# Kernel tuning notes

Measured on AMD Instinct MI355X. Metric: run time of the kernel, lower is better.

Reference implementation:

```python
import jax, jax.numpy as jnp
import numpy as np

EPS = 1e-6

def _layernorm(x, g, b):
    mu = jnp.mean(x, axis=-1, keepdims=True)
    var = jnp.mean(jnp.square(x - mu), axis=-1, keepdims=True)
    return (x - mu) * jax.lax.rsqrt(var + EPS) * g + b

def _mhsa(xq, xk, xv, mask, Wq, bq, Wk, bk, Wv, bv, Wo, bo, num_heads):
    B, Nq, D = xq.shape
    Nk = xk.shape[1]
    dh = D // num_heads
    # project then split heads: [B, N, D] -> [B, H, N, dh]
    def split(x, W, b, N):
        return (x @ W + b).reshape(B, N, num_heads, dh).transpose(0, 2, 1, 3)
    q = split(xq, Wq, bq, Nq)
    k = split(xk, Wk, bk, Nk)
    v = split(xv, Wv, bv, Nk)
    scores = jnp.einsum('bhnd,bhmd->bhnm', q, k) / jnp.sqrt(jnp.float32(dh))
    if mask is not None:
        scores = scores + mask * (-1e9)
    w = jax.nn.softmax(scores, axis=-1)
    out = jnp.einsum('bhnm,bhmd->bhnd', w, v)          # [B,H,Nq,dh]
    out = out.transpose(0, 2, 1, 3).reshape(B, Nq, D)  # concat heads
    return out @ Wo + bo

def setup_inputs() -> dict:
    B, N, D, FF = 2, 2048, 512, 2048
    key = jax.random.key(0)
    ks = jax.random.split(key, 32)
    std = 0.02
    p = {}
    p['inputs'] = jax.random.normal(ks[0], (B, N, D), jnp.float32)
    p['enc_output'] = jax.random.normal(ks[1], (B, N, D), jnp.float32)
    # causal look-ahead mask: 1 where masked (future positions)
    p['look_ahead_mask'] = jnp.triu(jnp.ones((N, N), jnp.float32), k=1)[None, None]
    p['padding_mask'] = jnp.zeros((B, 1, 1, N), jnp.float32)
    i = 2
    for pre in ('q1', 'k1', 'v1', 'o1', 'q2', 'k2', 'v2', 'o2'):
        p[pre + '_w'] = jax.random.normal(ks[i], (D, D), jnp.float32) * std; i += 1
        p[pre + '_b'] = jnp.zeros((D,), jnp.float32)
    p['f1_w'] = jax.random.normal(ks[i], (D, FF), jnp.float32) * std; i += 1
    p['f1_b'] = jnp.zeros((FF,), jnp.float32)
    p['f2_w'] = jax.random.normal(ks[i], (FF, D), jnp.float32) * std; i += 1
    p['f2_b'] = jnp.zeros((D,), jnp.float32)
    for ln in ('ln1', 'ln2', 'ln3'):
        p[ln + '_g'] = jnp.ones((D,), jnp.float32)
        p[ln + '_b'] = jnp.zeros((D,), jnp.float32)
    p['training'] = 0
    return p

def reference(inputs, enc_output, look_ahead_mask, padding_mask,
              q1_w, q1_b, k1_w, k1_b, v1_w, v1_b, o1_w, o1_b,
              q2_w, q2_b, k2_w, k2_b, v2_w, v2_b, o2_w, o2_b,
              f1_w, f1_b, f2_w, f2_b,
              ln1_g, ln1_b, ln2_g, ln2_b, ln3_g, ln3_b,
              training):
    H = 8
    # self-attention (q=k=v=inputs), causal mask; dropout inactive (eval)
    attn1 = _mhsa(inputs, inputs, inputs, look_ahead_mask,
                  q1_w, q1_b, k1_w, k1_b, v1_w, v1_b, o1_w, o1_b, H)
    out1 = _layernorm(inputs + attn1, ln1_g, ln1_b)
    # cross attention: NOTE original arg order -> q=enc, k=enc, v=out1
    attn2 = _mhsa(enc_output, enc_output, out1, padding_mask,
                  q2_w, q2_b, k2_w, k2_b, v2_w, v2_b, o2_w, o2_b, H)
    out2 = _layernorm(out1 + attn2, ln2_g, ln2_b)
    ffn = jax.nn.relu(out2 @ f1_w + f1_b) @ f2_w + f2_b
    return _layernorm(out2 + ffn, ln3_g, ln3_b)
```

## Files before the change

### kernel.cpp

```cpp
#include <hip/hip_runtime.h>

typedef __attribute__((ext_vector_type(8))) _Float16 half8;
typedef __attribute__((ext_vector_type(4))) _Float16 half4;
typedef __attribute__((ext_vector_type(2))) _Float16 half2_t;
typedef __attribute__((ext_vector_type(2))) __fp16 fp16x2;
typedef __attribute__((ext_vector_type(4))) float f32x4;

#define AS1 __attribute__((address_space(1)))
#define AS3 __attribute__((address_space(3)))

constexpr int SEQ = 2048, DM = 512, FFD = 2048, NH = 8, DH = 64;
constexpr int M = 2 * SEQ;
constexpr float QSCALE = 0.125f * 1.4426950408889634f;

__global__ __launch_bounds__(256)
void preproc(const float* __restrict__ q1_w, const float* __restrict__ k1_w,
             const float* __restrict__ v1_w, const float* __restrict__ o1_w,
             const float* __restrict__ q2_w, const float* __restrict__ k2_w,
             const float* __restrict__ v2_w, const float* __restrict__ o2_w,
             const float* __restrict__ f1_w, const float* __restrict__ f2_w,
             _Float16* __restrict__ qk1t, _Float16* __restrict__ v1t,
             _Float16* __restrict__ o1t, _Float16* __restrict__ qk2t,
             _Float16* __restrict__ v2t, _Float16* __restrict__ o2t,
             _Float16* __restrict__ f1t, _Float16* __restrict__ f2t,
             const float* __restrict__ q1_b, const float* __restrict__ k1_b,
             const float* __restrict__ q2_b, const float* __restrict__ k2_b,
             float* __restrict__ qk1b, float* __restrict__ qk2b,
             const float* __restrict__ inp, const float* __restrict__ enc,
             _Float16* __restrict__ xh, _Float16* __restrict__ eh) {
    __shared__ _Float16 tile[64 * 65];
    const int j = blockIdx.x, tid = threadIdx.x;
    if (j < 1024) {
        const float* src; _Float16* dst; int K, N, n0, k0;
        if (j < 512) {
            int w8 = j >> 6, t = j & 63;
            K = 512; N = 512; n0 = (t & 7) * 64; k0 = (t >> 3) * 64;
            switch (w8) {
                case 0: src = q1_w; dst = qk1t; break;
                case 1: src = k1_w; dst = qk1t + 512 * 512; break;
                case 2: src = v1_w; dst = v1t; break;
                case 3: src = o1_w; dst = o1t; break;
                case 4: src = q2_w; dst = qk2t; break;
                case 5: src = k2_w; dst = qk2t + 512 * 512; break;
                case 6: src = v2_w; dst = v2t; break;
                default: src = o2_w; dst = o2t; break;
            }
        } else if (j < 768) {
            int t = j - 512; K = 512; N = 2048;
            n0 = (t % 32) * 64; k0 = (t / 32) * 64; src = f1_w; dst = f1t;
        } else {
            int t = j - 768; K = 2048; N = 512;
            n0 = (t % 8) * 64; k0 = (t / 8) * 64; src = f2_w; dst = f2t;
        }
        int c = tid & 63, r4 = tid >> 6;
        for (int i = 0; i < 16; i++) {
            int r = r4 * 16 + i;
            tile[r * 65 + c] = (_Float16)src[(size_t)(k0 + r) * N + n0 + c];
        }
        __syncthreads();
        for (int i = 0; i < 16; i++) {
            int r = r4 * 16 + i;
            dst[(size_t)(n0 + r) * K + k0 + c] = tile[c * 65 + r];
        }
    } else if (j == 1024) {
        for (int i = tid; i < 512; i += 256) { qk1b[i] = q1_b[i]; qk1b[512 + i] = k1_b[i]; }
    } else if (j == 1025) {
        for (int i = tid; i < 512; i += 256) { qk2b[i] = q2_b[i]; qk2b[512 + i] = k2_b[i]; }
    } else {
        int k = j - 1026;
        const float* s = (k < 1024) ? inp : enc;
        _Float16* d = (k < 1024) ? xh : eh;
        size_t base = (size_t)(k & 1023) * 2048 + tid * 8;
        f32x4 a = *(const f32x4*)(s + base);
        f32x4 b2 = *(const f32x4*)(s + base + 4);
        half8 h;
        h[0] = (_Float16)a[0]; h[1] = (_Float16)a[1];
        h[2] = (_Float16)a[2]; h[3] = (_Float16)a[3];
        h[4] = (_Float16)b2[0]; h[5] = (_Float16)b2[1];
        h[6] = (_Float16)b2[2]; h[7] = (_Float16)b2[3];
        *(half8*)(d + base) = h;
    }
}

template<int BM, int BN, int WM, int WN, bool RELU, int EPI, int SPLIT>
__global__ __launch_bounds__(256)
void gemm_tn(const _Float16* __restrict__ A, const _Float16* __restrict__ Bt,
             const float* __restrict__ bias,
             float* __restrict__ outF, _Float16* __restrict__ outH,
             _Float16* __restrict__ Qh, _Float16* __restrict__ Kh,
             const _Float16* __restrict__ A2, const _Float16* __restrict__ Bt2,
             const float* __restrict__ bias2,
             _Float16* __restrict__ Qh2, _Float16* __restrict__ Kh2,
             int Mtot, int N, int K) {
    constexpr int ROWS = BM + BN;
    __shared__ _Float16 smem[ROWS * 64];
    constexpr int AF = WM / 16, BF = WN / 16;
    constexpr int WROW = BM / WM;
    const int tid = threadIdx.x;
    const int wid = tid >> 6, lid = tid & 63;
    const int wr = (wid % WROW) * WM;
    const int wc = (wid / WROW) * WN;
    const int mi = lid & 15, qd = lid >> 4;
    const int gx = gridDim.x, gy = gridDim.y;
    const int L = blockIdx.y * gx + blockIdx.x;
    const int by = L % gy, bx = L / gy;
    const int m0 = by * BM, n0 = bx * BN;
    const int Kc = K / SPLIT;
    const int kbase = (SPLIT > 1) ? blockIdx.z * Kc : 0;
    const int job = (EPI == 4) ? blockIdx.z : 0;
    const _Float16* Ap = ((EPI == 4 && job) ? A2 : A) + (size_t)m0 * K + kbase;
    const _Float16* Bp = ((EPI == 4 && job) ? Bt2 : Bt) + (size_t)n0 * K + kbase;
    const float* bsel = (EPI == 4 && job) ? bias2 : bias;
    const int lrow = lid >> 3;
    const int gblk = (lid & 7) ^ ((lid >> 3) & 7);
    auto stage = [&](int kt) {
        #pragma unroll
        for (int l = 0; l < BM / 32; l++) {
            int c = l * 4 + wid;
            int row = c * 8 + lrow;
            __builtin_amdgcn_global_load_lds(
                (const AS1 unsigned int*)(Ap + (size_t)row * K + kt * 64 + gblk * 8),
                (AS3 unsigned int*)&smem[c * 512], 16, 0, 0);
        }
        #pragma unroll
        for (int l = 0; l < BN / 32; l++) {
            int c = l * 4 + wid;
            int row = c * 8 + lrow;
            __builtin_amdgcn_global_load_lds(
                (const AS1 unsigned int*)(Bp + (size_t)row * K + kt * 64 + gblk * 8),
                (AS3 unsigned int*)&smem[BM * 64 + c * 512], 16, 0, 0);
        }
    };
    f32x4 acc[AF][BF] = {};
    const int NIT = Kc / 64;
    stage(0);
    __builtin_amdgcn_s_waitcnt(0x0F70);
    __syncthreads();
    for (int t = 0; t < NIT; t++) {
        #pragma unroll
        for (int h = 0; h < 2; h++) {
            const int sA = ((4 * h + qd) ^ (mi & 7)) * 8;
            half8 af[AF], bfr[BF];
            #pragma unroll
            for (int i = 0; i < AF; i++)
                af[i] = *(const half8*)&smem[(wr + i * 16 + mi) * 64 + sA];
            #pragma unroll
            for (int j = 0; j < BF; j++)
                bfr[j] = *(const half8*)&smem[(BM + wc + j * 16 + mi) * 64 + sA];
            #pragma unroll
            for (int i = 0; i < AF; i++)
                #pragma unroll
                for (int j = 0; j < BF; j++)
                    acc[i][j] = __builtin_amdgcn_mfma_f32_16x16x32_f16(af[i], bfr[j], acc[i][j], 0, 0, 0);
        }
        if (t + 1 < NIT) {
            __syncthreads();
            stage(t + 1);
            __builtin_amdgcn_s_waitcnt(0x0F70);
            __syncthreads();
        }
    }
    float* oF = outF;
    if (SPLIT > 1 && outF) oF = outF + (size_t)blockIdx.z * Mtot * N;
    _Float16* oH = outH;
    if (EPI == 5) oH = outH + (size_t)blockIdx.z * Mtot * N;
    const bool doBias = bsel && (SPLIT == 1 || blockIdx.z == 0);
    #pragma unroll
    for (int i = 0; i < AF; i++) {
        #pragma unroll
        for (int j = 0; j < BF; j++) {
            #pragma unroll
            for (int r = 0; r < 4; r++) {
                int row = m0 + wr + i * 16 + qd * 4 + r;
                int col = n0 + wc + j * 16 + mi;
                float v = acc[i][j][r];
                if (EPI == 3) {
                    v += bsel[row];
                    outH[(size_t)row * N + col] = (_Float16)v;
                } else if (EPI == 4) {
                    if (doBias) v += bsel[col];
                    int hh = (col >> 6) & 7, d = col & 63;
                    int bb = row >> 11, n = row & 2047;
                    size_t idx = (((size_t)bb * 8 + hh) * SEQ + n) * 64 + d;
                    if (col < 512) (job ? Qh2 : Qh)[idx] = (_Float16)(v * QSCALE);
                    else           (job ? Kh2 : Kh)[idx] = (_Float16)v;
                } else if (EPI == 5) {
                    if (doBias) v += bsel[col];
                    oH[(size_t)row * N + col] = (_Float16)v;
                } else {
                    if (doBias) v += bsel[col];
                    if (RELU) v = fmaxf(v, 0.f);
                    size_t off = (size_t)row * N + col;
                    if (oF) oF[off] = v;
                    if (outH) outH[off] = (_Float16)v;
                }
            }
        }
    }
}

template<bool CAUSAL>
__global__ __launch_bounds__(256)
void attn_chunk(const _Float16* __restrict__ Qh, const _Float16* __restrict__ Kh,
                const _Float16* __restrict__ VT, int ldv,
                _Float16* __restrict__ Opart, float* __restrict__ Lpart) {
    const int qt = blockIdx.x, bh = blockIdx.y, c = blockIdx.z;
    int t0, stp, n;
    if (CAUSAL) {
        if (c > qt) return;
        t0 = c; stp = 4; n = (qt - c) / 4 + 1;
    } else {
        t0 = c * 8; stp = 1; n = 8;
    }
    __shared__ _Float16 QPs[64 * 64];
    __shared__ _Float16 Ks[2][64 * 64];
    __shared__ _Float16 Vs[2][64 * 64];
    const int tid = threadIdx.x, w = tid >> 6, lane = tid & 63;
    const int mi = lane & 15, qd = lane >> 4;
    const int qbase = qt * 64;
    const int b = bh >> 3, h = bh & 7;
    const _Float16* Qp = Qh + ((size_t)bh * SEQ + qbase) * 64;
    const _Float16* Kp = Kh + (size_t)bh * SEQ * 64;
    const _Float16* Vp = VT + (size_t)(h * 64) * ldv + (size_t)b * SEQ;
    const int r0 = tid >> 3, blk = tid & 7;
    const int sw = (blk ^ (r0 & 7)) * 8;
    const int lrow = lane >> 3;
    const int gblk = (lane & 7) ^ ((lane >> 3) & 7);
    const int f0 = (qd ^ (mi & 7)) * 8;
    const int f1 = ((qd + 4) ^ (mi & 7)) * 8;

    {
        half8 q0 = *(const half8*)(Qp + r0 * 64 + blk * 8);
        half8 q1 = *(const half8*)(Qp + (r0 + 32) * 64 + blk * 8);
        *(half8*)&QPs[r0 * 64 + sw] = q0;
        *(half8*)&QPs[(r0 + 32) * 64 + sw] = q1;
    }
    auto stageKV = [&](int t, int buf) {
        #pragma unroll
        for (int l = 0; l < 2; l++) {
            int cc = l * 4 + w;
            int row = cc * 8 + lrow;
            __builtin_amdgcn_global_load_lds(
                (const AS1 unsigned int*)(Kp + ((size_t)(t * 64 + row)) * 64 + gblk * 8),
                (AS3 unsigned int*)&Ks[buf][cc * 512], 16, 0, 0);
            __builtin_amdgcn_global_load_lds(
                (const AS1 unsigned int*)(Vp + (size_t)row * ldv + t * 64 + gblk * 8),
                (AS3 unsigned int*)&Vs[buf][cc * 512], 16, 0, 0);
        }
    };
    stageKV(t0, 0);
    __builtin_amdgcn_s_waitcnt(0x0F70);
    __syncthreads();
    half8 qb0 = *(half8*)&QPs[(w * 16 + mi) * 64 + f0];
    half8 qb1 = *(half8*)&QPs[(w * 16 + mi) * 64 + f1];
    f32x4 oacc[4] = {};
    float lacc = 0.f;
    for (int i = 0; i < n; i++) {
        const int t = t0 + i * stp;
        if (i + 1 < n) stageKV(t0 + (i + 1) * stp, (i + 1) & 1);
        const _Float16* ksb = Ks[i & 1];
        const _Float16* vsb = Vs[i & 1];
        f32x4 s[4];
        #pragma unroll
        for (int j = 0; j < 4; j++) {
            half8 ka0 = *(const half8*)&ksb[(j * 16 + mi) * 64 + f0];
            half8 ka1 = *(const half8*)&ksb[(j * 16 + mi) * 64 + f1];
            f32x4 a = {};
            a = __builtin_amdgcn_mfma_f32_16x16x32_f16(ka0, qb0, a, 0, 0, 0);
            a = __builtin_amdgcn_mfma_f32_16x16x32_f16(ka1, qb1, a, 0, 0, 0);
            s[j] = a;
        }
        if (CAUSAL && t == qt) {
            int qg = qbase + w * 16 + mi;
            #pragma unroll
            for (int j = 0; j < 4; j++)
                #pragma unroll
                for (int r = 0; r < 4; r++) {
                    int key = t * 64 + j * 16 + qd * 4 + r;
                    if (key > qg) s[j][r] = -1e30f;
                }
        }
        #pragma unroll
        for (int j = 0; j < 4; j++)
            #pragma unroll
            for (int r = 0; r < 4; r++) {
                float pv = __builtin_amdgcn_exp2f(s[j][r]);
                s[j][r] = pv;
                lacc += pv;
            }
        #pragma unroll
        for (int j = 0; j < 4; j++) {
            fp16x2 lo = __builtin_amdgcn_cvt_pkrtz(s[j][0], s[j][1]);
            fp16x2 hi = __builtin_amdgcn_cvt_pkrtz(s[j][2], s[j][3]);
            half2_t lo2 = __builtin_bit_cast(half2_t, lo);
            half2_t hi2 = __builtin_bit_cast(half2_t, hi);
            half4 pq;
            pq[0] = lo2[0]; pq[1] = lo2[1]; pq[2] = hi2[0]; pq[3] = hi2[1];
            int blkp = (2 * j + (qd >> 1)) ^ (mi & 7);
            *(half4*)&QPs[(w * 16 + mi) * 64 + blkp * 8 + (qd & 1) * 4] = pq;
        }
        half8 pa0 = *(half8*)&QPs[(w * 16 + mi) * 64 + f0];
        half8 pa1 = *(half8*)&QPs[(w * 16 + mi) * 64 + f1];
        #pragma unroll
        for (int j = 0; j < 4; j++) {
            half8 vb0 = *(const half8*)&vsb[(j * 16 + mi) * 64 + f0];
            half8 vb1 = *(const half8*)&vsb[(j * 16 + mi) * 64 + f1];
            oacc[j] = __builtin_amdgcn_mfma_f32_16x16x32_f16(pa0, vb0, oacc[j], 0, 0, 0);
            oacc[j] = __builtin_amdgcn_mfma_f32_16x16x32_f16(pa1, vb1, oacc[j], 0, 0, 0);
        }
        __builtin_amdgcn_s_waitcnt(0x0F70);
        __syncthreads();
    }
    const size_t tb = (((size_t)c * 16 + bh) * 32 + qt) * 4096;
    #pragma unroll
    for (int j = 0; j < 4; j++)
        #pragma unroll
        for (int r = 0; r < 4; r++)
            Opart[tb + (size_t)(w * 16 + qd * 4 + r) * 64 + j * 16 + mi] = (_Float16)oacc[j][r];
    lacc += __shfl_xor(lacc, 16, 64);
    lacc += __shfl_xor(lacc, 32, 64);
    if (qd == 0)
        Lpart[(((size_t)c * 16 + bh) * 32 + qt) * 64 + w * 16 + mi] = lacc;
}

template<bool CAUSAL>
__global__ __launch_bounds__(256)
void attn_combine(const _Float16* __restrict__ Opart, const float* __restrict__ Lpart,
                  _Float16* __restrict__ O) {
    const int qt = blockIdx.x, bh = blockIdx.y;
    const int b = bh >> 3, h = bh & 7;
    const int NC = CAUSAL ? min(qt + 1, 4) : 4;
    const int d = threadIdx.x & 63;
    const int rr = threadIdx.x >> 6;
    for (int it = 0; it < 16; it++) {
        int q = it * 4 + rr;
        float lsum = 0.f, acc = 0.f;
        for (int cc = 0; cc < NC; cc++) {
            lsum += Lpart[(((size_t)cc * 16 + bh) * 32 + qt) * 64 + q];
            acc += (float)Opart[(((size_t)cc * 16 + bh) * 32 + qt) * 4096 + (size_t)q * 64 + d];
        }
        int qrow = qt * 64 + q;
        O[((size_t)(b * SEQ + qrow)) * 512 + h * 64 + d] = (_Float16)(acc / lsum);
    }
}

template<typename RT>
__global__ __launch_bounds__(256)
void add_ln(const RT* __restrict__ res, const _Float16* __restrict__ y,
            size_t pstride, int nparts,
            const float* __restrict__ g, const float* __restrict__ bb,
            float* __restrict__ outF, _Float16* __restrict__ outH) {
    int row = blockIdx.x;
    int tid = threadIdx.x;
    size_t base = (size_t)row * 512;
    float x0 = (float)res[base + tid];
    float x1 = (float)res[base + tid + 256];
    for (int s = 0; s < nparts; s++) {
        x0 += (float)y[s * pstride + base + tid];
        x1 += (float)y[s * pstride + base + tid + 256];
    }
    float s = x0 + x1, sq = x0 * x0 + x1 * x1;
    #pragma unroll
    for (int off = 32; off > 0; off >>= 1) {
        s += __shfl_xor(s, off, 64);
        sq += __shfl_xor(sq, off, 64);
    }
    __shared__ float ls[4], lq[4];
    int w = tid >> 6;
    if ((tid & 63) == 0) { ls[w] = s; lq[w] = sq; }
    __syncthreads();
    s = ls[0] + ls[1] + ls[2] + ls[3];
    sq = lq[0] + lq[1] + lq[2] + lq[3];
    float mu = s * (1.f / 512.f);
    float var = sq * (1.f / 512.f) - mu * mu;
    float rs = rsqrtf(var + 1e-6f);
    float o0 = (x0 - mu) * rs * g[tid] + bb[tid];
    float o1 = (x1 - mu) * rs * g[tid + 256] + bb[tid + 256];
    if (outF) { outF[base + tid] = o0; outF[base + tid + 256] = o1; }
    if (outH) { outH[base + tid] = (_Float16)o0; outH[base + tid + 256] = (_Float16)o1; }
}

extern "C" void kernel_launch(void* const* d_in, const int* in_sizes, int n_in,
                              void* d_out, int out_size, void* d_ws, size_t ws_size,
                              hipStream_t stream) {
    (void)in_sizes; (void)n_in; (void)out_size; (void)ws_size;
    const float* inp  = (const float*)d_in[0];
    const float* enc  = (const float*)d_in[1];
    const float* q1_w = (const float*)d_in[4];
    const float* q1_b = (const float*)d_in[5];
    const float* k1_w = (const float*)d_in[6];
    const float* k1_b = (const float*)d_in[7];
    const float* v1_w = (const float*)d_in[8];
    const float* v1_b = (const float*)d_in[9];
    const float* o1_w = (const float*)d_in[10];
    const float* o1_b = (const float*)d_in[11];
    const float* q2_w = (const float*)d_in[12];
    const float* q2_b = (const float*)d_in[13];
    const float* k2_w = (const float*)d_in[14];
    const float* k2_b = (const float*)d_in[15];
    const float* v2_w = (const float*)d_in[16];
    const float* v2_b = (const float*)d_in[17];
    const float* o2_w = (const float*)d_in[18];
    const float* o2_b = (const float*)d_in[19];
    const float* f1_w = (const float*)d_in[20];
    const float* f1_b = (const float*)d_in[21];
    const float* f2_w = (const float*)d_in[22];
    const float* f2_b = (const float*)d_in[23];
    const float* ln1_g = (const float*)d_in[24];
    const float* ln1_b = (const float*)d_in[25];
    const float* ln2_g = (const float*)d_in[26];
    const float* ln2_b = (const float*)d_in[27];
    const float* ln3_g = (const float*)d_in[28];
    const float* ln3_b = (const float*)d_in[29];

    char* p = (char*)d_ws;
    auto alloc = [&](size_t bytes) { char* r = p; p += (bytes + 255) & ~(size_t)255; return (void*)r; };
    _Float16* xh    = (_Float16*)alloc((size_t)M * DM * 2);
    _Float16* eh    = (_Float16*)alloc((size_t)M * DM * 2);
    _Float16* qk1t  = (_Float16*)alloc((size_t)1024 * DM * 2);
    _Float16* v1t   = (_Float16*)alloc((size_t)DM * DM * 2);
    _Float16* o1t   = (_Float16*)alloc((size_t)DM * DM * 2);
    _Float16* qk2t  = (_Float16*)alloc((size_t)1024 * DM * 2);
    _Float16* v2t   = (_Float16*)alloc((size_t)DM * DM * 2);
    _Float16* o2t   = (_Float16*)alloc((size_t)DM * DM * 2);
    _Float16* f1t   = (_Float16*)alloc((size_t)FFD * DM * 2);
    _Float16* f2t   = (_Float16*)alloc((size_t)DM * FFD * 2);
    float* qk1b     = (float*)alloc(1024 * 4);
    float* qk2b     = (float*)alloc(1024 * 4);
    _Float16* Qh1   = (_Float16*)alloc((size_t)M * DM * 2);
    _Float16* Kh1   = (_Float16*)alloc((size_t)M * DM * 2);
    _Float16* Qh2   = (_Float16*)alloc((size_t)M * DM * 2);
    _Float16* Kh2   = (_Float16*)alloc((size_t)M * DM * 2);
    _Float16* V1T   = (_Float16*)alloc((size_t)DM * M * 2);
    _Float16* V2T   = (_Float16*)alloc((size_t)DM * M * 2);
    _Float16* Ah    = (_Float16*)alloc((size_t)M * DM * 2);
    _Float16* Ph    = (_Float16*)alloc((size_t)2 * M * DM * 2);
    float* Lbuf     = (float*)alloc((size_t)4 * 16 * 32 * 64 * 4);
    _Float16* out1h = (_Float16*)alloc((size_t)M * DM * 2);
    _Float16* out2h = (_Float16*)alloc((size_t)M * DM * 2);
    _Float16* hh    = (_Float16*)alloc((size_t)M * FFD * 2);
    _Float16* OpH   = (_Float16*)alloc((size_t)4 * 16 * 32 * 4096 * 2);
    const size_t PS = (size_t)M * DM;

    dim3 t256(256);
    preproc<<<dim3(1026 + 2048), t256, 0, stream>>>(
        q1_w, k1_w, v1_w, o1_w, q2_w, k2_w, v2_w, o2_w, f1_w, f2_w,
        qk1t, v1t, o1t, qk2t, v2t, o2t, f1t, f2t,
        q1_b, k1_b, q2_b, k2_b, qk1b, qk2b, inp, enc, xh, eh);

    gemm_tn<128, 128, 64, 64, false, 4, 1><<<dim3(8, 32, 2), t256, 0, stream>>>(
        xh, qk1t, qk1b, nullptr, nullptr, Qh1, Kh1,
        eh, qk2t, qk2b, Qh2, Kh2, M, 1024, 512);
    gemm_tn<64, 64, 32, 32, false, 3, 1><<<dim3(64, 8), t256, 0, stream>>>(
        v1t, xh, v1_b, nullptr, V1T, nullptr, nullptr,
        nullptr, nullptr, nullptr, nullptr, nullptr, 512, M, 512);

    attn_chunk<true><<<dim3(32, 16, 4), t256, 0, stream>>>(Qh1, Kh1, V1T, M, OpH, Lbuf);
    attn_combine<true><<<dim3(32, 16), t256, 0, stream>>>(OpH, Lbuf, Ah);
    gemm_tn<64, 64, 32, 32, false, 5, 2><<<dim3(8, 64, 2), t256, 0, stream>>>(
        Ah, o1t, o1_b, nullptr, Ph, nullptr, nullptr,
        nullptr, nullptr, nullptr, nullptr, nullptr, M, 512, 512);
    add_ln<float><<<dim3(M), t256, 0, stream>>>(inp, Ph, PS, 2, ln1_g, ln1_b, nullptr, out1h);

    gemm_tn<64, 64, 32, 32, false, 3, 1><<<dim3(64, 8), t256, 0, stream>>>(
        v2t, out1h, v2_b, nullptr, V2T, nullptr, nullptr,
        nullptr, nullptr, nullptr, nullptr, nullptr, 512, M, 512);
    attn_chunk<false><<<dim3(32, 16, 4), t256, 0, stream>>>(Qh2, Kh2, V2T, M, OpH, Lbuf);
    attn_combine<false><<<dim3(32, 16), t256, 0, stream>>>(OpH, Lbuf, Ah);
    gemm_tn<64, 64, 32, 32, false, 5, 2><<<dim3(8, 64, 2), t256, 0, stream>>>(
        Ah, o2t, o2_b, nullptr, Ph, nullptr, nullptr,
        nullptr, nullptr, nullptr, nullptr, nullptr, M, 512, 512);
    add_ln<_Float16><<<dim3(M), t256, 0, stream>>>(out1h, Ph, PS, 2, ln2_g, ln2_b, nullptr, out2h);

    gemm_tn<128, 128, 64, 64, true, 0, 1><<<dim3(16, 32), t256, 0, stream>>>(
        out2h, f1t, f1_b, nullptr, hh, nullptr, nullptr,
        nullptr, nullptr, nullptr, nullptr, nullptr, M, 2048, 512);
    gemm_tn<64, 128, 32, 64, false, 5, 2><<<dim3(4, 64, 2), t256, 0, stream>>>(
        hh, f2t, f2_b, nullptr, Ph, nullptr, nullptr,
        nullptr, nullptr, nullptr, nullptr, nullptr, M, 512, 2048);
    add_ln<_Float16><<<dim3(M), t256, 0, stream>>>(out2h, Ph, PS, 2, ln3_g, ln3_b, (float*)d_out, nullptr);
}
```

Baseline: 344.8 us.

## Fuse attention combine and add+layernorm into producers via last-block atomic counters

New measurement: 1.286 ms. 273% more time.

```diff
diff --git a/kernel.cpp b/kernel.cpp
--- a/kernel.cpp
+++ b/kernel.cpp
@@ -27,7 +27,8 @@
              const float* __restrict__ q2_b, const float* __restrict__ k2_b,
              float* __restrict__ qk1b, float* __restrict__ qk2b,
              const float* __restrict__ inp, const float* __restrict__ enc,
-             _Float16* __restrict__ xh, _Float16* __restrict__ eh) {
+             _Float16* __restrict__ xh, _Float16* __restrict__ eh,
+             int* __restrict__ cnts) {
     __shared__ _Float16 tile[64 * 65];
     const int j = blockIdx.x, tid = threadIdx.x;
     if (j < 1024) {
@@ -66,7 +67,7 @@
         for (int i = tid; i < 512; i += 256) { qk1b[i] = q1_b[i]; qk1b[512 + i] = k1_b[i]; }
     } else if (j == 1025) {
         for (int i = tid; i < 512; i += 256) { qk2b[i] = q2_b[i]; qk2b[512 + i] = k2_b[i]; }
-    } else {
+    } else if (j < 3074) {
         int k = j - 1026;
         const float* s = (k < 1024) ? inp : enc;
         _Float16* d = (k < 1024) ? xh : eh;
@@ -79,10 +80,12 @@
         h[4] = (_Float16)b2[0]; h[5] = (_Float16)b2[1];
         h[6] = (_Float16)b2[2]; h[7] = (_Float16)b2[3];
         *(half8*)(d + base) = h;
+    } else {
+        for (int i = tid; i < 1216; i += 256) cnts[i] = 0;
     }
 }
 
-template<int BM, int BN, int WM, int WN, bool RELU, int EPI, int SPLIT>
+template<int BM, int BN, int WM, int WN, bool RELU, int EPI, int SPLIT, typename RT>
 __global__ __launch_bounds__(256)
 void gemm_tn(const _Float16* __restrict__ A, const _Float16* __restrict__ Bt,
              const float* __restrict__ bias,
@@ -91,6 +94,10 @@
              const _Float16* __restrict__ A2, const _Float16* __restrict__ Bt2,
              const float* __restrict__ bias2,
              _Float16* __restrict__ Qh2, _Float16* __restrict__ Kh2,
+             const RT* __restrict__ res, const float* __restrict__ lng,
+             const float* __restrict__ lnb,
+             float* __restrict__ lnF, _Float16* __restrict__ lnH,
+             int* __restrict__ cnt,
              int Mtot, int N, int K) {
     constexpr int ROWS = BM + BN;
     __shared__ _Float16 smem[ROWS * 64];
@@ -197,13 +204,55 @@
             }
         }
     }
+    if constexpr (EPI == 5) {
+        __threadfence();
+        __shared__ int lastf;
+        if (tid == 0) {
+            int prev = atomicAdd(&cnt[by], 1);
+            lastf = (prev == (int)(gridDim.x * gridDim.z) - 1);
+        }
+        __syncthreads();
+        if (!lastf) return;
+        __threadfence();
+        const int lane2 = tid & 63, wv = tid >> 6;
+        const _Float16* P0 = outH;
+        const _Float16* P1 = outH + (size_t)Mtot * N;
+        for (int r = wv; r < BM; r += 4) {
+            size_t rbase = (size_t)(m0 + r) * N;
+            float x[8];
+            float ssum = 0.f, sqsum = 0.f;
+            #pragma unroll
+            for (int e = 0; e < 8; e++) {
+                int c2 = lane2 + e * 64;
+                float xv = (float)res[rbase + c2] + (float)P0[rbase + c2]
+                         + (float)P1[rbase + c2];
+                x[e] = xv; ssum += xv; sqsum += xv * xv;
+            }
+            #pragma unroll
+            for (int off = 32; off > 0; off >>= 1) {
+                ssum += __shfl_xor(ssum, off, 64);
+                sqsum += __shfl_xor(sqsum, off, 64);
+            }
+            float mu = ssum * (1.f / 512.f);
+            float var = sqsum * (1.f / 512.f) - mu * mu;
+            float rs = rsqrtf(var + 1e-6f);
+            #pragma unroll
+            for (int e = 0; e < 8; e++) {
+                int c2 = lane2 + e * 64;
+                float o = (x[e] - mu) * rs * lng[c2] + lnb[c2];
+                if (lnF) lnF[rbase + c2] = o;
+                if (lnH) lnH[rbase + c2] = (_Float16)o;
+            }
+        }
+    }
 }
 
 template<bool CAUSAL>
 __global__ __launch_bounds__(256)
 void attn_chunk(const _Float16* __restrict__ Qh, const _Float16* __restrict__ Kh,
                 const _Float16* __restrict__ VT, int ldv,
-                _Float16* __restrict__ Opart, float* __restrict__ Lpart) {
+                _Float16* __restrict__ Opart, float* __restrict__ Lpart,
+                _Float16* __restrict__ O, int* __restrict__ cnt) {
     const int qt = blockIdx.x, bh = blockIdx.y, c = blockIdx.z;
     int t0, stp, n;
     if (CAUSAL) {
@@ -321,63 +370,28 @@
     lacc += __shfl_xor(lacc, 32, 64);
     if (qd == 0)
         Lpart[(((size_t)c * 16 + bh) * 32 + qt) * 64 + w * 16 + mi] = lacc;
-}
-
-template<bool CAUSAL>
-__global__ __launch_bounds__(256)
-void attn_combine(const _Float16* __restrict__ Opart, const float* __restrict__ Lpart,
-                  _Float16* __restrict__ O) {
-    const int qt = blockIdx.x, bh = blockIdx.y;
-    const int b = bh >> 3, h = bh & 7;
+
+    __threadfence();
+    __shared__ int lastc;
+    if (tid == 0) {
+        int NCt = CAUSAL ? min(qt + 1, 4) : 4;
+        int prev = atomicAdd(&cnt[qt * 16 + bh], 1);
+        lastc = (prev == NCt - 1);
+    }
+    __syncthreads();
+    if (!lastc) return;
+    __threadfence();
     const int NC = CAUSAL ? min(qt + 1, 4) : 4;
-    const int d = threadIdx.x & 63;
-    const int rr = threadIdx.x >> 6;
+    const int d = tid & 63, rr = tid >> 6;
     for (int it = 0; it < 16; it++) {
         int q = it * 4 + rr;
-        float lsum = 0.f, acc = 0.f;
+        float lsum = 0.f, av = 0.f;
         for (int cc = 0; cc < NC; cc++) {
             lsum += Lpart[(((size_t)cc * 16 + bh) * 32 + qt) * 64 + q];
-            acc += (float)Opart[(((size_t)cc * 16 + bh) * 32 + qt) * 4096 + (size_t)q * 64 + d];
-        }
-        int qrow = qt * 64 + q;
-        O[((size_t)(b * SEQ + qrow)) * 512 + h * 64 + d] = (_Float16)(acc / lsum);
-    }
-}
-
-template<typename RT>
-__global__ __launch_bounds__(256)
-void add_ln(const RT* __restrict__ res, const _Float16* __restrict__ y,
-            size_t pstride, int nparts,
-            const float* __restrict__ g, const float* __restrict__ bb,
-            float* __restrict__ outF, _Float16* __restrict__ outH) {
-    int row = blockIdx.x;
-    int tid = threadIdx.x;
-    size_t base = (size_t)row * 512;
-    float x0 = (float)res[base + tid];
-    float x1 = (float)res[base + tid + 256];
-    for (int s = 0; s < nparts; s++) {
-        x0 += (float)y[s * pstride + base + tid];
-        x1 += (float)y[s * pstride + base + tid + 256];
-    }
-    float s = x0 + x1, sq = x0 * x0 + x1 * x1;
-    #pragma unroll
-    for (int off = 32; off > 0; off >>= 1) {
-        s += __shfl_xor(s, off, 64);
-        sq += __shfl_xor(sq, off, 64);
-    }
-    __shared__ float ls[4], lq[4];
-    int w = tid >> 6;
-    if ((tid & 63) == 0) { ls[w] = s; lq[w] = sq; }
-    __syncthreads();
-    s = ls[0] + ls[1] + ls[2] + ls[3];
-    sq = lq[0] + lq[1] + lq[2] + lq[3];
-    float mu = s * (1.f / 512.f);
-    float var = sq * (1.f / 512.f) - mu * mu;
-    float rs = rsqrtf(var + 1e-6f);
-    float o0 = (x0 - mu) * rs * g[tid] + bb[tid];
-    float o1 = (x1 - mu) * rs * g[tid + 256] + bb[tid + 256];
-    if (outF) { outF[base + tid] = o0; outF[base + tid + 256] = o1; }
-    if (outH) { outH[base + tid] = (_Float16)o0; outH[base + tid + 256] = (_Float16)o1; }
+            av += (float)Opart[(((size_t)cc * 16 + bh) * 32 + qt) * 4096 + (size_t)q * 64 + d];
+        }
+        O[((size_t)(b * SEQ + qt * 64 + q)) * 512 + h * 64 + d] = (_Float16)(av / lsum);
+    }
 }
 
 extern "C" void kernel_launch(void* const* d_in, const int* in_sizes, int n_in,
@@ -440,43 +454,54 @@
     _Float16* out2h = (_Float16*)alloc((size_t)M * DM * 2);
     _Float16* hh    = (_Float16*)alloc((size_t)M * FFD * 2);
     _Float16* OpH   = (_Float16*)alloc((size_t)4 * 16 * 32 * 4096 * 2);
-    const size_t PS = (size_t)M * DM;
+    int* cnts       = (int*)alloc(1216 * 4);
 
     dim3 t256(256);
-    preproc<<<dim3(1026 + 2048), t256, 0, stream>>>(
+    preproc<<<dim3(3075), t256, 0, stream>>>(
         q1_w, k1_w, v1_w, o1_w, q2_w, k2_w, v2_w, o2_w, f1_w, f2_w,
         qk1t, v1t, o1t, qk2t, v2t, o2t, f1t, f2t,
-        q1_b, k1_b, q2_b, k2_b, qk1b, qk2b, inp, enc, xh, eh);
-
-    gemm_tn<128, 128, 64, 64, false, 4, 1><<<dim3(8, 32, 2), t256, 0, stream>>>(
+        q1_b, k1_b, q2_b, k2_b, qk1b, qk2b, inp, enc, xh, eh, cnts);
+
+    gemm_tn<128, 64, 64, 32, false, 4, 1, float><<<dim3(16, 32, 2), t256, 0, stream>>>(
         xh, qk1t, qk1b, nullptr, nullptr, Qh1, Kh1,
-        eh, qk2t, qk2b, Qh2, Kh2, M, 1024, 512);
-    gemm_tn<64, 64, 32, 32, false, 3, 1><<<dim3(64, 8), t256, 0, stream>>>(
+        eh, qk2t, qk2b, Qh2, Kh2,
+        nullptr, nullptr, nullptr, nullptr, nullptr, nullptr,
+        M, 1024, 512);
+    gemm_tn<64, 64, 32, 32, false, 3, 1, float><<<dim3(64, 8), t256, 0, stream>>>(
         v1t, xh, v1_b, nullptr, V1T, nullptr, nullptr,
-        nullptr, nullptr, nullptr, nullptr, nullptr, 512, M, 512);
-
-    attn_chunk<true><<<dim3(32, 16, 4), t256, 0, stream>>>(Qh1, Kh1, V1T, M, OpH, Lbuf);
-    attn_combine<true><<<dim3(32, 16), t256, 0, stream>>>(OpH, Lbuf, Ah);
-    gemm_tn<64, 64, 32, 32, false, 5, 2><<<dim3(8, 64, 2), t256, 0, stream>>>(
+        nullptr, nullptr, nullptr, nullptr, nullptr,
+        nullptr, nullptr, nullptr, nullptr, nullptr, nullptr,
+        512, M, 512);
+
+    attn_chunk<true><<<dim3(32, 16, 4), t256, 0, stream>>>(
+        Qh1, Kh1, V1T, M, OpH, Lbuf, Ah, cnts);
+    gemm_tn<64, 64, 32, 32, false, 5, 2, float><<<dim3(8, 64, 2), t256, 0, stream>>>(
         Ah, o1t, o1_b, nullptr, Ph, nullptr, nullptr,
-        nullptr, nullptr, nullptr, nullptr, nullptr, M, 512, 512);
-    add_ln<float><<<dim3(M), t256, 0, stream>>>(inp, Ph, PS, 2, ln1_g, ln1_b, nullptr, out1h);
-
-    gemm_tn<64, 64, 32, 32, false, 3, 1><<<dim3(64, 8), t256, 0, stream>>>(
+        nullptr, nullptr, nullptr, nullptr, nullptr,
+        inp, ln1_g, ln1_b, nullptr, out1h, cnts + 1024,
+        M, 512, 512);
+
+    gemm_tn<64, 64, 32, 32, false, 3, 1, float><<<dim3(64, 8), t256, 0, stream>>>(
         v2t, out1h, v2_b, nullptr, V2T, nullptr, nullptr,
-        nullptr, nullptr, nullptr, nullptr, nullptr, 512, M, 512);
-    attn_chunk<false><<<dim3(32, 16, 4), t256, 0, stream>>>(Qh2, Kh2, V2T, M, OpH, Lbuf);
-    attn_combine<false><<<dim3(32, 16), t256, 0, stream>>>(OpH, Lbuf, Ah);
-    gemm_tn<64, 64, 32, 32, false, 5, 2><<<dim3(8, 64, 2), t256, 0, stream>>>(
+        nullptr, nullptr, nullptr, nullptr, nullptr,
+        nullptr, nullptr, nullptr, nullptr, nullptr, nullptr,
+        512, M, 512);
+    attn_chunk<false><<<dim3(32, 16, 4), t256, 0, stream>>>(
+        Qh2, Kh2, V2T, M, OpH, Lbuf, Ah, cnts + 512);
+    gemm_tn<64, 64, 32, 32, false, 5, 2, _Float16><<<dim3(8, 64, 2), t256, 0, stream>>>(
         Ah, o2t, o2_b, nullptr, Ph, nullptr, nullptr,
-        nullptr, nullptr, nullptr, nullptr, nullptr, M, 512, 512);
-    add_ln<_Float16><<<dim3(M), t256, 0, stream>>>(out1h, Ph, PS, 2, ln2_g, ln2_b, nullptr, out2h);
-
-    gemm_tn<128, 128, 64, 64, true, 0, 1><<<dim3(16, 32), t256, 0, stream>>>(
+        nullptr, nullptr, nullptr, nullptr, nullptr,
+        out1h, ln2_g, ln2_b, nullptr, out2h, cnts + 1088,
+        M, 512, 512);
+
+    gemm_tn<128, 64, 64, 32, true, 0, 1, float><<<dim3(32, 32), t256, 0, stream>>>(
         out2h, f1t, f1_b, nullptr, hh, nullptr, nullptr,
-        nullptr, nullptr, nullptr, nullptr, nullptr, M, 2048, 512);
-    gemm_tn<64, 128, 32, 64, false, 5, 2><<<dim3(4, 64, 2), t256, 0, stream>>>(
+        nullptr, nullptr, nullptr, nullptr, nullptr,
+        nullptr, nullptr, nullptr, nullptr, nullptr, nullptr,
+        M, 2048, 512);
+    gemm_tn<64, 64, 32, 32, false, 5, 2, _Float16><<<dim3(8, 64, 2), t256, 0, stream>>>(
         hh, f2t, f2_b, nullptr, Ph, nullptr, nullptr,
-        nullptr, nullptr, nullptr, nullptr, nullptr, M, 512, 2048);
-    add_ln<_Float16><<<dim3(M), t256, 0, stream>>>(out2h, Ph, PS, 2, ln3_g, ln3_b, (float*)d_out, nullptr);
+        nullptr, nullptr, nullptr, nullptr, nullptr,
+        out2h, ln3_g, ln3_b, (float*)d_out, nullptr, cnts + 1152,
+        M, 512, 2048);
 }
```
